# Kernel optimization log

Measured on AMD Instinct MI355X. Metric: run time of the kernel, lower is better.

The kernel has to match this reference:

```python
import jax, jax.numpy as jnp
import numpy as np

HIDDEN = 768
NUM_HEADS = 12
HEAD_DIM = HIDDEN // NUM_HEADS
WINDOW = 128
NEG = -1e30  # stand-in for -inf that is safe under autodiff


def setup_inputs() -> dict:
    key = jax.random.key(0)
    ks = jax.random.split(key, 12)
    B, S = 2, 2048
    hidden = jax.random.normal(ks[0], (B, S, HIDDEN), dtype=jnp.float32)
    attention_mask = jnp.ones((B, S), dtype=jnp.int32)
    global_mask = jax.random.randint(ks[1], (B, S), 0, 2, dtype=jnp.int32)
    def lin(kw, kb):
        W = jax.random.normal(kw, (HIDDEN, HIDDEN), dtype=jnp.float32) * 0.02
        b = jax.random.normal(kb, (HIDDEN,), dtype=jnp.float32) * 0.02
        return W, b
    Wq, bq = lin(ks[2], ks[3])
    Wk, bk = lin(ks[4], ks[5])
    Wv, bv = lin(ks[6], ks[7])
    Wo, bo = lin(ks[8], ks[9])
    return {"hidden": hidden, "attention_mask": attention_mask, "global_mask": global_mask,
            "Wq": Wq, "bq": bq, "Wk": Wk, "bk": bk, "Wv": Wv, "bv": bv, "Wo": Wo, "bo": bo}


def _attend(hidden, attention_mask, global_mask, Wq, bq, Wk, bk, Wv, bv, Wo, bo):
    B, S, H = hidden.shape
    def proj(W, b):
        # (B,S,H) -> (B,nh,S,hd); nn.Linear computes x @ W.T + b
        return (hidden @ W.T + b).reshape(B, S, NUM_HEADS, HEAD_DIM).transpose(0, 2, 1, 3)
    q, k, v = proj(Wq, bq), proj(Wk, bk), proj(Wv, bv)
    scale = jnp.asarray(np.sqrt(HEAD_DIM), dtype=hidden.dtype)
    scores = jnp.einsum('bhqd,bhkd->bhqk', q, k) / scale  # (B,nh,S,S)
    # sliding window mask: |i-j| <= WINDOW
    idx = jnp.arange(S)
    window = (jnp.abs(idx[:, None] - idx[None, :]) <= WINDOW)  # (S,S)
    g = global_mask.astype(bool)
    combined = window[None] | g[:, :, None] | g[:, None, :]     # (B,S,S)
    combined = combined & attention_mask.astype(bool)[:, None, :]  # pad mask on keys
    scores = jnp.where(combined[:, None, :, :], scores, NEG)
    attn = jax.nn.softmax(scores, axis=-1)
    # torch code zeroes NaN rows (fully masked); replicate safely
    attn = jnp.where(jnp.isnan(attn), 0.0, attn)
    out = jnp.einsum('bhqk,bhkd->bhqd', attn, v)  # (B,nh,S,hd)
    out = out.transpose(0, 2, 1, 3).reshape(B, S, H)
    return out @ Wo.T + bo


def reference(hidden, attention_mask, global_mask, Wq, bq, Wk, bk, Wv, bv, Wo, bo):
    return _attend(hidden, attention_mask, global_mask, Wq, bq, Wk, bk, Wv, bv, Wo, bo)
```

## Files before the change

kernel.cpp:

```cpp
#include <hip/hip_runtime.h>
#include <math.h>

#define S_LEN 2048
#define HID   768
#define NH    12
#define HD    64
#define WIN   128
#define NEGV  (-1e30f)
#define QSCALE 0.1803368801111204f

typedef __attribute__((ext_vector_type(8))) short short8v;
typedef __attribute__((ext_vector_type(4))) float float4v;
typedef unsigned short u16;

__device__ __forceinline__ u16 f2bf(float f) {
    union { float f; unsigned int u; } c; c.f = f;
    unsigned int u = c.u + 0x7FFFu + ((c.u >> 16) & 1u);
    return (u16)(u >> 16);
}

__device__ __forceinline__ short8v cvt8(float4 a, float4 b) {
    short8v t;
    t[0]=(short)f2bf(a.x); t[1]=(short)f2bf(a.y); t[2]=(short)f2bf(a.z); t[3]=(short)f2bf(a.w);
    t[4]=(short)f2bf(b.x); t[5]=(short)f2bf(b.y); t[6]=(short)f2bf(b.z); t[7]=(short)f2bf(b.w);
    return t;
}

__device__ __forceinline__ unsigned int pk2bf(float a, float b) {
    unsigned int r;
    asm("v_cvt_pk_bf16_f32 %0, %1, %2" : "=v"(r) : "v"(a), "v"(b));
    return r;
}

__device__ __forceinline__ float exp2_fast(float x) {
    float r;
    asm("v_exp_f32 %0, %1" : "=v"(r) : "v"(x));
    return r;
}

__device__ __forceinline__ void gload_lds16(const void* g, void* l) {
    __builtin_amdgcn_global_load_lds(
        (const __attribute__((address_space(1))) unsigned int*)g,
        (__attribute__((address_space(3))) unsigned int*)l, 16, 0, 0);
}

__global__ __launch_bounds__(256) void convert_inputs(
    const float* __restrict__ hidden, const float* __restrict__ Wq,
    const float* __restrict__ Wk, const float* __restrict__ Wv,
    const float* __restrict__ Wo, u16* __restrict__ hbf, u16* __restrict__ w4)
{
    const int y = blockIdx.y;
    const float* src; u16* dst; int n; float scale = 1.f;
    if (y == 0) { src = hidden; dst = hbf; n = 4096*HID; }
    else {
        src = (y==1) ? Wq : (y==2) ? Wk : (y==3) ? Wv : Wo;
        dst = w4 + (size_t)(y-1)*HID*HID;
        n = HID*HID;
        if (y == 1) scale = QSCALE;
    }
    const int idx = (blockIdx.x*256 + threadIdx.x) * 8;
    if (idx >= n) return;
    float4 f0 = *(const float4*)(src + idx);
    float4 f1 = *(const float4*)(src + idx + 4);
    f0.x*=scale; f0.y*=scale; f0.z*=scale; f0.w*=scale;
    f1.x*=scale; f1.y*=scale; f1.z*=scale; f1.w*=scale;
    *(short8v*)(dst + idx) = cvt8(f0, f1);
}

__global__ __launch_bounds__(256) void gemm_mfma(
    const u16* __restrict__ A, const u16* __restrict__ W4,
    const float* __restrict__ bA, const float* __restrict__ bB,
    const float* __restrict__ bC, u16* __restrict__ obf,
    u16* __restrict__ ovt, float* __restrict__ of32, int mode)
{
    __shared__ __align__(16) u16 As[128*32];
    __shared__ __align__(16) u16 Bs[128*32];

    const int tid = threadIdx.x;
    const int w = tid >> 6, l = tid & 63;
    const int lx = l & 15, lg = l >> 4;
    const int wr = w >> 1, wc = w & 1;
    const int m0 = blockIdx.x * 128, n0 = blockIdx.y * 128;
    const int z = (mode == 0) ? blockIdx.z : 3;
    const float* bias = (mode == 1) ? bA : (z == 0 ? bA : (z == 1 ? bB : bC));
    const float bscale = (mode == 0 && z == 0) ? QSCALE : 1.0f;
    const u16* Wp = W4 + (size_t)z * (HID*HID);

    float4v acc[4][4];
    const float4v fz = {0.f,0.f,0.f,0.f};
    #pragma unroll
    for (int i = 0; i < 4; i++)
        #pragma unroll
        for (int j = 0; j < 4; j++) acc[i][j] = fz;

    for (int kt = 0; kt < HID/32; kt++) {
        const int k0 = kt * 32;
        __syncthreads();
        #pragma unroll
        for (int rnd = 0; rnd < 2; rnd++) {
            const int ch  = rnd*256 + w*64 + l;
            const int row = ch >> 2, kc = ch & 3;
            gload_lds16(A  + (size_t)(m0+row)*HID + k0 + kc*8,
                        As + (size_t)(rnd*256 + w*64)*8);
            gload_lds16(Wp + (size_t)(n0+row)*HID + k0 + kc*8,
                        Bs + (size_t)(rnd*256 + w*64)*8);
        }
        __syncthreads();
        short8v af[4], bfr[4];
        #pragma unroll
        for (int i = 0; i < 4; i++) {
            af[i]  = *(const short8v*)(As + (wr*64 + i*16 + lx)*32 + lg*8);
            bfr[i] = *(const short8v*)(Bs + (wc*64 + i*16 + lx)*32 + lg*8);
        }
        #pragma unroll
        for (int i = 0; i < 4; i++)
            #pragma unroll
            for (int j = 0; j < 4; j++)
                acc[i][j] = __builtin_amdgcn_mfma_f32_16x16x32_bf16(af[i], bfr[j], acc[i][j], 0, 0, 0);
    }

    #pragma unroll
    for (int j = 0; j < 4; j++) {
        const int col = n0 + wc*64 + j*16 + lx;
        const float bval = bias[col] * bscale;
        const int hh = col >> 6, d = col & 63;
        #pragma unroll
        for (int i = 0; i < 4; i++) {
            const int rbase = m0 + wr*64 + i*16 + lg*4;
            const int bb = rbase >> 11, s = rbase & 2047;
            const float v0 = acc[i][j][0] + bval;
            const float v1 = acc[i][j][1] + bval;
            const float v2 = acc[i][j][2] + bval;
            const float v3 = acc[i][j][3] + bval;
            if (mode == 1) {
                of32[(size_t)(rbase+0)*HID + col] = v0;
                of32[(size_t)(rbase+1)*HID + col] = v1;
                of32[(size_t)(rbase+2)*HID + col] = v2;
                of32[(size_t)(rbase+3)*HID + col] = v3;
            } else if (z == 2) {
                uint2 ow; ow.x = pk2bf(v0, v1); ow.y = pk2bf(v2, v3);
                *(uint2*)&ovt[(((size_t)bb*NH + hh)*HD + d)*S_LEN + s] = ow;
            } else {
                u16* base = obf + (size_t)z * ((size_t)2*S_LEN*HID);
                base[(((size_t)bb*NH + hh)*S_LEN + s+0)*HD + d] = f2bf(v0);
                base[(((size_t)bb*NH + hh)*S_LEN + s+1)*HD + d] = f2bf(v1);
                base[(((size_t)bb*NH + hh)*S_LEN + s+2)*HD + d] = f2bf(v2);
                base[(((size_t)bb*NH + hh)*S_LEN + s+3)*HD + d] = f2bf(v3);
            }
        }
    }
}

__global__ __launch_bounds__(256) void attn_mfma(
    const u16* __restrict__ Q, const u16* __restrict__ K,
    const u16* __restrict__ Vt, const int* __restrict__ amask,
    const int* __restrict__ gmask, u16* __restrict__ AO)
{
    __shared__ __align__(16) u16 Ks[64*64];
    __shared__ __align__(16) u16 Vs[64*64];
    __shared__ __align__(16) u16 Ps[4*16*64];
    __shared__ __align__(16) float fA[64];
    __shared__ __align__(16) float fB[64];

    const int tid = threadIdx.x;
    const int w  = tid >> 6;
    const int l  = tid & 63;
    const int lx = l & 15;
    const int lg = l >> 4;
    const int b  = blockIdx.z;
    const int h  = blockIdx.y;
    const int q0 = blockIdx.x * 64;
    const size_t bh = ((size_t)b*NH + h) * S_LEN;

    const int q_glob = q0 + w*16 + lx;

    short8v aq[2];
    {
        const u16* qp = Q + (bh + q_glob)*HD + lg*8;
        aq[0] = *(const short8v*)(qp);
        aq[1] = *(const short8v*)(qp + 32);
    }
    const int gq = gmask[(size_t)b*S_LEN + q_glob];
    const float* fP = gq ? fA : fB;

    float m_i = NEGV, l_i = 0.f;
    float4v o_acc[4];
    const float4v fzv = {0.f, 0.f, 0.f, 0.f};
    #pragma unroll
    for (int db = 0; db < 4; db++) o_acc[db] = fzv;

    const int str = tid >> 2;
    const int stc = tid & 3;
    const int rb  = str * 128;
    const int sw  = (str & 7) << 4;
    const u16* Kbase = K + bh * HD;
    const u16* Vbase = Vt + (size_t)(b*NH + h) * HD * S_LEN;
    const int psw = (lx & 7) << 4;

    for (int kt = 0; kt < S_LEN/64; kt++) {
        const int k0 = kt * 64;
        __syncthreads();
        {
            const u16* kp = Kbase + (size_t)(k0 + str)*HD + stc*16;
            uint4 u0 = *(const uint4*)(kp);
            uint4 u1 = *(const uint4*)(kp + 8);
            *(uint4*)((char*)Ks + rb + ((stc*32)      ^ sw)) = u0;
            *(uint4*)((char*)Ks + rb + ((stc*32 + 16) ^ sw)) = u1;
        }
        {
            const u16* vp = Vbase + (size_t)str*S_LEN + k0 + stc*16;
            uint4 u0 = *(const uint4*)(vp);
            uint4 u1 = *(const uint4*)(vp + 8);
            *(uint4*)((char*)Vs + rb + ((stc*32)      ^ sw)) = u0;
            *(uint4*)((char*)Vs + rb + ((stc*32 + 16) ^ sw)) = u1;
        }
        if (tid < 64) {
            const int am = amask[(size_t)b*S_LEN + k0 + tid];
            const int gk = gmask[(size_t)b*S_LEN + k0 + tid];
            fA[tid] = am ? 0.f : NEGV;
            fB[tid] = (am && gk) ? 0.f : NEGV;
        }
        __syncthreads();

        float4v sacc[4];
        #pragma unroll
        for (int kb = 0; kb < 4; kb++) sacc[kb] = fzv;
        #pragma unroll
        for (int kb = 0; kb < 4; kb++) {
            const int key = kb*16 + lx;
            const int ksw = (key & 7) << 4;
            #pragma unroll
            for (int ks = 0; ks < 2; ks++) {
                short8v bk = *(const short8v*)((char*)Ks + key*128 + ((16*lg + 64*ks) ^ ksw));
                sacc[kb] = __builtin_amdgcn_mfma_f32_16x16x32_bf16(bk, aq[ks], sacc[kb], 0, 0, 0);
            }
        }

        float sv[4][4];
        const int adq = (k0 > q0) ? (k0 - q0) : (q0 - k0);
        if (adq <= 64) {
            #pragma unroll
            for (int kb = 0; kb < 4; kb++) {
                float4 fa4 = *(const float4*)&fA[kb*16 + lg*4];
                sv[kb][0] = sacc[kb][0] + fa4.x;
                sv[kb][1] = sacc[kb][1] + fa4.y;
                sv[kb][2] = sacc[kb][2] + fa4.z;
                sv[kb][3] = sacc[kb][3] + fa4.w;
            }
        } else if (adq >= 192) {
            #pragma unroll
            for (int kb = 0; kb < 4; kb++) {
                float4 fp4 = *(const float4*)&fP[kb*16 + lg*4];
                sv[kb][0] = sacc[kb][0] + fp4.x;
                sv[kb][1] = sacc[kb][1] + fp4.y;
                sv[kb][2] = sacc[kb][2] + fp4.z;
                sv[kb][3] = sacc[kb][3] + fp4.w;
            }
        } else {
            #pragma unroll
            for (int kb = 0; kb < 4; kb++) {
                float4 fa4 = *(const float4*)&fA[kb*16 + lg*4];
                float4 fb4 = *(const float4*)&fB[kb*16 + lg*4];
                const int e = q_glob - (k0 + kb*16 + lg*4);
                #pragma unroll
                for (int r = 0; r < 4; r++) {
                    int dd = e - r; dd = dd < 0 ? -dd : dd;
                    const bool wing = (dd <= WIN) || gq;
                    const float fa = (&fa4.x)[r], fb = (&fb4.x)[r];
                    sv[kb][r] = sacc[kb][r] + (wing ? fa : fb);
                }
            }
        }

        float mloc;
        {
            float t0 = fmaxf(fmaxf(sv[0][0], sv[0][1]), fmaxf(sv[0][2], sv[0][3]));
            float t1 = fmaxf(fmaxf(sv[1][0], sv[1][1]), fmaxf(sv[1][2], sv[1][3]));
            float t2 = fmaxf(fmaxf(sv[2][0], sv[2][1]), fmaxf(sv[2][2], sv[2][3]));
            float t3 = fmaxf(fmaxf(sv[3][0], sv[3][1]), fmaxf(sv[3][2], sv[3][3]));
            mloc = fmaxf(fmaxf(t0, t1), fmaxf(t2, t3));
        }
        mloc = fmaxf(mloc, __shfl_xor(mloc, 16));
        mloc = fmaxf(mloc, __shfl_xor(mloc, 32));
        if (__any(mloc > m_i + 8.0f)) {
            const float mnew = fmaxf(m_i, mloc);
            const float sc = exp2_fast(m_i - mnew);
            l_i *= sc;
            #pragma unroll
            for (int db = 0; db < 4; db++)
                #pragma unroll
                for (int r = 0; r < 4; r++) o_acc[db][r] *= sc;
            m_i = mnew;
        }
        float p[4][4];
        float lsum = 0.f;
        #pragma unroll
        for (int kb = 0; kb < 4; kb++)
            #pragma unroll
            for (int r = 0; r < 4; r++) {
                p[kb][r] = exp2_fast(sv[kb][r] - m_i);
                lsum += p[kb][r];
            }
        lsum += __shfl_xor(lsum, 16);
        lsum += __shfl_xor(lsum, 32);
        l_i += lsum;

        #pragma unroll
        for (int kb = 0; kb < 4; kb++) {
            uint2 pw;
            pw.x = pk2bf(p[kb][0], p[kb][1]);
            pw.y = pk2bf(p[kb][2], p[kb][3]);
            *(uint2*)((char*)Ps + w*2048 + lx*128 + ((kb*32 + lg*8) ^ psw)) = pw;
        }

        #pragma unroll
        for (int ks = 0; ks < 2; ks++) {
            short8v pa = *(const short8v*)((char*)Ps + w*2048 + lx*128 +
                                           ((16*lg + 64*ks) ^ psw));
            #pragma unroll
            for (int db = 0; db < 4; db++) {
                const int drow = db*16 + lx;
                short8v bv = *(const short8v*)((char*)Vs + drow*128 +
                                               ((16*lg + 64*ks) ^ ((drow & 7) << 4)));
                o_acc[db] = __builtin_amdgcn_mfma_f32_16x16x32_bf16(bv, pa, o_acc[db], 0, 0, 0);
            }
        }
    }

    {
        const float inv = 1.f / l_i;
        u16* op = AO + ((size_t)b*S_LEN + q_glob)*HID + h*HD + lg*4;
        #pragma unroll
        for (int db = 0; db < 4; db++) {
            uint2 ow;
            ow.x = pk2bf(o_acc[db][0]*inv, o_acc[db][1]*inv);
            ow.y = pk2bf(o_acc[db][2]*inv, o_acc[db][3]*inv);
            *(uint2*)(op + db*16) = ow;
        }
    }
}

extern "C" void kernel_launch(void* const* d_in, const int* in_sizes, int n_in,
                              void* d_out, int out_size, void* d_ws, size_t ws_size,
                              hipStream_t stream)
{
    const float* hidden = (const float*)d_in[0];
    const int*   amask  = (const int*)d_in[1];
    const int*   gmask  = (const int*)d_in[2];
    const float* Wq = (const float*)d_in[3];
    const float* bq = (const float*)d_in[4];
    const float* Wk = (const float*)d_in[5];
    const float* bk = (const float*)d_in[6];
    const float* Wv = (const float*)d_in[7];
    const float* bv = (const float*)d_in[8];
    const float* Wo = (const float*)d_in[9];
    const float* bo = (const float*)d_in[10];
    float* out = (float*)d_out;

    char* ws = (char*)d_ws;
    const size_t NTOK = (size_t)2 * S_LEN * HID;
    u16* hbf   = (u16*)(ws);
    u16* w4    = (u16*)(ws + 6291456);
    u16* qkvbf = (u16*)(ws + 11010048);
    u16* vtbf  = (u16*)(ws + 29884416);
    u16* aobf  = (u16*)(ws + 36175872);

    convert_inputs<<<dim3(1536, 5), 256, 0, stream>>>(hidden, Wq, Wk, Wv, Wo, hbf, w4);

    gemm_mfma<<<dim3(32, 6, 3), 256, 0, stream>>>(hbf, w4, bq, bk, bv, qkvbf, vtbf, nullptr, 0);

    u16* Qbf = qkvbf;
    u16* Kbf = qkvbf + NTOK;

    attn_mfma<<<dim3(S_LEN/64, NH, 2), 256, 0, stream>>>(Qbf, Kbf, vtbf, amask, gmask, aobf);

    gemm_mfma<<<dim3(32, 6), 256, 0, stream>>>(aobf, w4, bo, nullptr, nullptr, nullptr, nullptr, out, 1);
}
```

Baseline: 112.5 us.

## Prefetch next K/V tile into registers with double-buffered LDS and swizzled block order

The attention kernel now loads the next 64-key K/V tile and its mask values into registers while the current tile is computed, then writes them into a second LDS buffer (ping-pong KsA/VsA and KsB/VsB). The aim is to hide global-load latency behind the MFMA and softmax work. The grid is flattened to 768 blocks with an XCD-style swizzle that maps consecutive blocks to the same (batch, head), which should improve L2 reuse of K/V. In exchange it doubles the K/V LDS footprint and adds register pressure, which may lower occupancy. The last iteration issues a redundant reload of the final tile.

```diff
diff --git a/kernel.cpp b/kernel.cpp
--- a/kernel.cpp
+++ b/kernel.cpp
@@ -156,8 +156,8 @@
     const u16* __restrict__ Vt, const int* __restrict__ amask,
     const int* __restrict__ gmask, u16* __restrict__ AO)
 {
-    __shared__ __align__(16) u16 Ks[64*64];
-    __shared__ __align__(16) u16 Vs[64*64];
+    __shared__ __align__(16) u16 KsA[64*64], VsA[64*64];
+    __shared__ __align__(16) u16 KsB[64*64], VsB[64*64];
     __shared__ __align__(16) u16 Ps[4*16*64];
     __shared__ __align__(16) float fA[64];
     __shared__ __align__(16) float fB[64];
@@ -167,9 +167,13 @@
     const int l  = tid & 63;
     const int lx = l & 15;
     const int lg = l >> 4;
-    const int b  = blockIdx.z;
-    const int h  = blockIdx.y;
-    const int q0 = blockIdx.x * 64;
+
+    const int bid = blockIdx.x;
+    const int swz = (bid & 7) * 96 + (bid >> 3);
+    const int q0 = (swz & 31) * 64;
+    const int hb = swz >> 5;
+    const int h  = hb % NH;
+    const int b  = hb / NH;
     const size_t bh = ((size_t)b*NH + h) * S_LEN;
 
     const int q_glob = q0 + w*16 + lx;
@@ -197,135 +201,160 @@
     const u16* Vbase = Vt + (size_t)(b*NH + h) * HD * S_LEN;
     const int psw = (lx & 7) << 4;
 
-    for (int kt = 0; kt < S_LEN/64; kt++) {
-        const int k0 = kt * 64;
+    uint4 rk0, rk1, rv0, rv1;
+    int ram = 0, rgk = 0;
+
+#define STAGE_REGS(KT) do {                                                   \
+    const int kk0_ = (KT) * 64;                                               \
+    const u16* kp_ = Kbase + (size_t)(kk0_ + str)*HD + stc*16;                \
+    rk0 = *(const uint4*)(kp_); rk1 = *(const uint4*)(kp_ + 8);               \
+    const u16* vp_ = Vbase + (size_t)str*S_LEN + kk0_ + stc*16;               \
+    rv0 = *(const uint4*)(vp_); rv1 = *(const uint4*)(vp_ + 8);               \
+    if (tid < 64) {                                                           \
+        ram = amask[(size_t)b*S_LEN + kk0_ + tid];                            \
+        rgk = gmask[(size_t)b*S_LEN + kk0_ + tid];                            \
+    }                                                                         \
+} while(0)
+
+#define WRITE_LDS(KS, VS) do {                                                \
+    *(uint4*)((char*)(KS) + rb + ((stc*32)      ^ sw)) = rk0;                 \
+    *(uint4*)((char*)(KS) + rb + ((stc*32 + 16) ^ sw)) = rk1;                 \
+    *(uint4*)((char*)(VS) + rb + ((stc*32)      ^ sw)) = rv0;                 \
+    *(uint4*)((char*)(VS) + rb + ((stc*32 + 16) ^ sw)) = rv1;                 \
+    if (tid < 64) {                                                           \
+        fA[tid] = ram ? 0.f : NEGV;                                           \
+        fB[tid] = (ram && rgk) ? 0.f : NEGV;                                  \
+    }                                                                         \
+} while(0)
+
+#define COMPUTE(KS, VS, K0) do {                                              \
+    float4v sacc[4];                                                          \
+    _Pragma("unroll")                                                         \
+    for (int kb = 0; kb < 4; kb++) sacc[kb] = fzv;                            \
+    _Pragma("unroll")                                                         \
+    for (int kb = 0; kb < 4; kb++) {                                          \
+        const int key_ = kb*16 + lx;                                          \
+        const int ksw_ = (key_ & 7) << 4;                                     \
+        _Pragma("unroll")                                                     \
+        for (int ks = 0; ks < 2; ks++) {                                      \
+            short8v bk_ = *(const short8v*)((char*)(KS) + key_*128 +          \
+                                            ((16*lg + 64*ks) ^ ksw_));        \
+            sacc[kb] = __builtin_amdgcn_mfma_f32_16x16x32_bf16(bk_, aq[ks],   \
+                                                          sacc[kb], 0, 0, 0); \
+        }                                                                     \
+    }                                                                         \
+    float sv[4][4];                                                           \
+    const int adq_ = ((K0) > q0) ? ((K0) - q0) : (q0 - (K0));                 \
+    if (adq_ <= 64) {                                                         \
+        _Pragma("unroll")                                                     \
+        for (int kb = 0; kb < 4; kb++) {                                      \
+            float4 fa4 = *(const float4*)&fA[kb*16 + lg*4];                   \
+            sv[kb][0] = sacc[kb][0] + fa4.x;                                  \
+            sv[kb][1] = sacc[kb][1] + fa4.y;                                  \
+            sv[kb][2] = sacc[kb][2] + fa4.z;                                  \
+            sv[kb][3] = sacc[kb][3] + fa4.w;                                  \
+        }                                                                     \
+    } else if (adq_ >= 192) {                                                 \
+        _Pragma("unroll")                                                     \
+        for (int kb = 0; kb < 4; kb++) {                                      \
+            float4 fp4 = *(const float4*)&fP[kb*16 + lg*4];                   \
+            sv[kb][0] = sacc[kb][0] + fp4.x;                                  \
+            sv[kb][1] = sacc[kb][1] + fp4.y;                                  \
+            sv[kb][2] = sacc[kb][2] + fp4.z;                                  \
+            sv[kb][3] = sacc[kb][3] + fp4.w;                                  \
+        }                                                                     \
+    } else {                                                                  \
+        _Pragma("unroll")                                                     \
+        for (int kb = 0; kb < 4; kb++) {                                      \
+            float4 fa4 = *(const float4*)&fA[kb*16 + lg*4];                   \
+            float4 fb4 = *(const float4*)&fB[kb*16 + lg*4];                   \
+            const int e_ = q_glob - ((K0) + kb*16 + lg*4);                    \
+            _Pragma("unroll")                                                 \
+            for (int r = 0; r < 4; r++) {                                     \
+                int dd_ = e_ - r; dd_ = dd_ < 0 ? -dd_ : dd_;                 \
+                const bool wing_ = (dd_ <= WIN) || gq;                        \
+                const float fa_ = (&fa4.x)[r], fb_ = (&fb4.x)[r];             \
+                sv[kb][r] = sacc[kb][r] + (wing_ ? fa_ : fb_);                \
+            }                                                                 \
+        }                                                                     \
+    }                                                                         \
+    float mloc;                                                               \
+    {                                                                         \
+        float t0 = fmaxf(fmaxf(sv[0][0], sv[0][1]), fmaxf(sv[0][2], sv[0][3]));\
+        float t1 = fmaxf(fmaxf(sv[1][0], sv[1][1]), fmaxf(sv[1][2], sv[1][3]));\
+        float t2 = fmaxf(fmaxf(sv[2][0], sv[2][1]), fmaxf(sv[2][2], sv[2][3]));\
+        float t3 = fmaxf(fmaxf(sv[3][0], sv[3][1]), fmaxf(sv[3][2], sv[3][3]));\
+        mloc = fmaxf(fmaxf(t0, t1), fmaxf(t2, t3));                           \
+    }                                                                         \
+    mloc = fmaxf(mloc, __shfl_xor(mloc, 16));                                 \
+    mloc = fmaxf(mloc, __shfl_xor(mloc, 32));                                 \
+    if (__any(mloc > m_i + 8.0f)) {                                           \
+        const float mnew_ = fmaxf(m_i, mloc);                                 \
+        const float sc_ = exp2_fast(m_i - mnew_);                             \
+        l_i *= sc_;                                                           \
+        _Pragma("unroll")                                                     \
+        for (int db = 0; db < 4; db++)                                        \
+            _Pragma("unroll")                                                 \
+            for (int r = 0; r < 4; r++) o_acc[db][r] *= sc_;                  \
+        m_i = mnew_;                                                          \
+    }                                                                         \
+    float p[4][4];                                                            \
+    float lsum = 0.f;                                                         \
+    _Pragma("unroll")                                                         \
+    for (int kb = 0; kb < 4; kb++)                                            \
+        _Pragma("unroll")                                                     \
+        for (int r = 0; r < 4; r++) {                                         \
+            p[kb][r] = exp2_fast(sv[kb][r] - m_i);                            \
+            lsum += p[kb][r];                                                 \
+        }                                                                     \
+    lsum += __shfl_xor(lsum, 16);                                             \
+    lsum += __shfl_xor(lsum, 32);                                             \
+    l_i += lsum;                                                              \
+    _Pragma("unroll")                                                         \
+    for (int kb = 0; kb < 4; kb++) {                                          \
+        uint2 pw;                                                             \
+        pw.x = pk2bf(p[kb][0], p[kb][1]);                                     \
+        pw.y = pk2bf(p[kb][2], p[kb][3]);                                     \
+        *(uint2*)((char*)Ps + w*2048 + lx*128 + ((kb*32 + lg*8) ^ psw)) = pw; \
+    }                                                                         \
+    _Pragma("unroll")                                                         \
+    for (int ks = 0; ks < 2; ks++) {                                          \
+        short8v pa_ = *(const short8v*)((char*)Ps + w*2048 + lx*128 +         \
+                                        ((16*lg + 64*ks) ^ psw));             \
+        _Pragma("unroll")                                                     \
+        for (int db = 0; db < 4; db++) {                                      \
+            const int drow_ = db*16 + lx;                                     \
+            short8v bv_ = *(const short8v*)((char*)(VS) + drow_*128 +         \
+                                    ((16*lg + 64*ks) ^ ((drow_ & 7) << 4)));  \
+            o_acc[db] = __builtin_amdgcn_mfma_f32_16x16x32_bf16(bv_, pa_,     \
+                                                          o_acc[db], 0, 0, 0);\
+        }                                                                     \
+    }                                                                         \
+} while(0)
+
+    STAGE_REGS(0);
+    WRITE_LDS(KsA, VsA);
+    __syncthreads();
+
+    for (int kt = 0; kt < S_LEN/64; kt += 2) {
+        STAGE_REGS(kt+1);
+        COMPUTE(KsA, VsA, kt*64);
+        __syncthreads();
+        WRITE_LDS(KsB, VsB);
         __syncthreads();
         {
-            const u16* kp = Kbase + (size_t)(k0 + str)*HD + stc*16;
-            uint4 u0 = *(const uint4*)(kp);
-            uint4 u1 = *(const uint4*)(kp + 8);
-            *(uint4*)((char*)Ks + rb + ((stc*32)      ^ sw)) = u0;
-            *(uint4*)((char*)Ks + rb + ((stc*32 + 16) ^ sw)) = u1;
+            const int kn = (kt+2 < S_LEN/64) ? (kt+2) : (S_LEN/64 - 1);
+            STAGE_REGS(kn);
         }
-        {
-            const u16* vp = Vbase + (size_t)str*S_LEN + k0 + stc*16;
-            uint4 u0 = *(const uint4*)(vp);
-            uint4 u1 = *(const uint4*)(vp + 8);
-            *(uint4*)((char*)Vs + rb + ((stc*32)      ^ sw)) = u0;
-            *(uint4*)((char*)Vs + rb + ((stc*32 + 16) ^ sw)) = u1;
-        }
-        if (tid < 64) {
-            const int am = amask[(size_t)b*S_LEN + k0 + tid];
-            const int gk = gmask[(size_t)b*S_LEN + k0 + tid];
-            fA[tid] = am ? 0.f : NEGV;
-            fB[tid] = (am && gk) ? 0.f : NEGV;
-        }
-        __syncthreads();
-
-        float4v sacc[4];
-        #pragma unroll
-        for (int kb = 0; kb < 4; kb++) sacc[kb] = fzv;
-        #pragma unroll
-        for (int kb = 0; kb < 4; kb++) {
-            const int key = kb*16 + lx;
-            const int ksw = (key & 7) << 4;
-            #pragma unroll
-            for (int ks = 0; ks < 2; ks++) {
-                short8v bk = *(const short8v*)((char*)Ks + key*128 + ((16*lg + 64*ks) ^ ksw));
-                sacc[kb] = __builtin_amdgcn_mfma_f32_16x16x32_bf16(bk, aq[ks], sacc[kb], 0, 0, 0);
-            }
-        }
-
-        float sv[4][4];
-        const int adq = (k0 > q0) ? (k0 - q0) : (q0 - k0);
-        if (adq <= 64) {
-            #pragma unroll
-            for (int kb = 0; kb < 4; kb++) {
-                float4 fa4 = *(const float4*)&fA[kb*16 + lg*4];
-                sv[kb][0] = sacc[kb][0] + fa4.x;
-                sv[kb][1] = sacc[kb][1] + fa4.y;
-                sv[kb][2] = sacc[kb][2] + fa4.z;
-                sv[kb][3] = sacc[kb][3] + fa4.w;
-            }
-        } else if (adq >= 192) {
-            #pragma unroll
-            for (int kb = 0; kb < 4; kb++) {
-                float4 fp4 = *(const float4*)&fP[kb*16 + lg*4];
-                sv[kb][0] = sacc[kb][0] + fp4.x;
-                sv[kb][1] = sacc[kb][1] + fp4.y;
-                sv[kb][2] = sacc[kb][2] + fp4.z;
-                sv[kb][3] = sacc[kb][3] + fp4.w;
-            }
-        } else {
-            #pragma unroll
-            for (int kb = 0; kb < 4; kb++) {
-                float4 fa4 = *(const float4*)&fA[kb*16 + lg*4];
-                float4 fb4 = *(const float4*)&fB[kb*16 + lg*4];
-                const int e = q_glob - (k0 + kb*16 + lg*4);
-                #pragma unroll
-                for (int r = 0; r < 4; r++) {
-                    int dd = e - r; dd = dd < 0 ? -dd : dd;
-                    const bool wing = (dd <= WIN) || gq;
-                    const float fa = (&fa4.x)[r], fb = (&fb4.x)[r];
-                    sv[kb][r] = sacc[kb][r] + (wing ? fa : fb);
-                }
-            }
-        }
-
-        float mloc;
-        {
-            float t0 = fmaxf(fmaxf(sv[0][0], sv[0][1]), fmaxf(sv[0][2], sv[0][3]));
-            float t1 = fmaxf(fmaxf(sv[1][0], sv[1][1]), fmaxf(sv[1][2], sv[1][3]));
-            float t2 = fmaxf(fmaxf(sv[2][0], sv[2][1]), fmaxf(sv[2][2], sv[2][3]));
-            float t3 = fmaxf(fmaxf(sv[3][0], sv[3][1]), fmaxf(sv[3][2], sv[3][3]));
-            mloc = fmaxf(fmaxf(t0, t1), fmaxf(t2, t3));
-        }
-        mloc = fmaxf(mloc, __shfl_xor(mloc, 16));
-        mloc = fmaxf(mloc, __shfl_xor(mloc, 32));
-        if (__any(mloc > m_i + 8.0f)) {
-            const float mnew = fmaxf(m_i, mloc);
-            const float sc = exp2_fast(m_i - mnew);
-            l_i *= sc;
-            #pragma unroll
-            for (int db = 0; db < 4; db++)
-                #pragma unroll
-                for (int r = 0; r < 4; r++) o_acc[db][r] *= sc;
-            m_i = mnew;
-        }
-        float p[4][4];
-        float lsum = 0.f;
-        #pragma unroll
-        for (int kb = 0; kb < 4; kb++)
-            #pragma unroll
-            for (int r = 0; r < 4; r++) {
-                p[kb][r] = exp2_fast(sv[kb][r] - m_i);
-                lsum += p[kb][r];
-            }
-        lsum += __shfl_xor(lsum, 16);
-        lsum += __shfl_xor(lsum, 32);
-        l_i += lsum;
-
-        #pragma unroll
-        for (int kb = 0; kb < 4; kb++) {
-            uint2 pw;
-            pw.x = pk2bf(p[kb][0], p[kb][1]);
-            pw.y = pk2bf(p[kb][2], p[kb][3]);
-            *(uint2*)((char*)Ps + w*2048 + lx*128 + ((kb*32 + lg*8) ^ psw)) = pw;
-        }
-
-        #pragma unroll
-        for (int ks = 0; ks < 2; ks++) {
-            short8v pa = *(const short8v*)((char*)Ps + w*2048 + lx*128 +
-                                           ((16*lg + 64*ks) ^ psw));
-            #pragma unroll
-            for (int db = 0; db < 4; db++) {
-                const int drow = db*16 + lx;
-                short8v bv = *(const short8v*)((char*)Vs + drow*128 +
-                                               ((16*lg + 64*ks) ^ ((drow & 7) << 4)));
-                o_acc[db] = __builtin_amdgcn_mfma_f32_16x16x32_bf16(bv, pa, o_acc[db], 0, 0, 0);
-            }
-        }
-    }
+        COMPUTE(KsB, VsB, (kt+1)*64);
+        __syncthreads();
+        WRITE_LDS(KsA, VsA);
+        __syncthreads();
+    }
+
+#undef STAGE_REGS
+#undef WRITE_LDS
+#undef COMPUTE
 
     {
         const float inv = 1.f / l_i;
@@ -372,7 +401,7 @@
     u16* Qbf = qkvbf;
     u16* Kbf = qkvbf + NTOK;
 
-    attn_mfma<<<dim3(S_LEN/64, NH, 2), 256, 0, stream>>>(Qbf, Kbf, vtbf, amask, gmask, aobf);
+    attn_mfma<<<dim3(768), 256, 0, stream>>>(Qbf, Kbf, vtbf, amask, gmask, aobf);
 
     gemm_mfma<<<dim3(32, 6), 256, 0, stream>>>(aobf, w4, bo, nullptr, nullptr, nullptr, nullptr, out, 1);
 }
```

Result: faster. 107.9 us (-4.0%).
